# Kernel optimization log

Hardware: AMD Instinct MI355X
Metric: run time of the kernel (lower is better)

## Reference

```python
import jax, jax.numpy as jnp
import numpy as np

EPS = 1e-6
SIGMA = 0.5          # observation_noise_std
E, B, M, C = 64, 512, 128, 128  # episode, batch, memory_size, code_size


def setup_inputs() -> dict:
    key = jax.random.key(0)
    k1, k2 = jax.random.split(key)
    return {
        "input_encoded": jax.random.normal(k1, (E, B, C), dtype=jnp.float32),
        "memory_mean": jax.random.normal(k2, (M, C), dtype=jnp.float32),
        "memory_logvar": jnp.zeros((1,), dtype=jnp.float32),
    }


def reference(input_encoded, memory_mean, memory_logvar):
    # GPM.write_to_memory with direct_writing=False (sequential Kalman write).
    bsz = input_encoded.shape[1]
    prior_var = jnp.exp(memory_logvar) * jnp.ones((M,), input_encoded.dtype) + EPS  # (M,)
    prior_mean = jnp.broadcast_to(memory_mean, (bsz, M, C))                # (B,M,C)
    prior_cov = jnp.broadcast_to(jnp.diag(prior_var), (bsz, M, M))         # (B,M,M)
    eye_m = jnp.eye(M, dtype=input_encoded.dtype)

    def step(carry, z_i):            # z_i: (B,C)
        mean, cov = carry            # (B,M,C), (B,M,M)
        # _solve_w_mean (pseudoinverse=False): w = inv(M M^T + s^2 I) M z
        gram = jnp.einsum('bmc,bnc->bmn', mean, mean) + (SIGMA ** 2) * eye_m
        mz = jnp.einsum('bmc,bc->bm', mean, z_i)
        w = jnp.linalg.solve(gram, mz[..., None])[..., 0]  # (B,M)
        # _update_memory: rank-1 Kalman update
        delta = z_i - jnp.einsum('bm,bmc->bc', w, mean)    # (B,C)
        wU = jnp.einsum('bm,bmn->bn', w, cov)              # (B,M)
        sig = jnp.sum(wU * w, axis=-1) + SIGMA ** 2        # (B,)
        c = wU / sig[:, None]                              # (B,M)
        new_mean = mean + c[:, :, None] * delta[:, None, :]
        new_cov = cov - c[:, :, None] * wU[:, None, :]
        return (new_mean, new_cov), None

    (post_mean, post_cov), _ = jax.lax.scan(step, (prior_mean, prior_cov), input_encoded)

    # _dkl_M
    p_diag = jnp.diagonal(prior_cov, axis1=-2, axis2=-1)   # (B,M)
    q_diag = jnp.diagonal(post_cov, axis1=-2, axis2=-1)    # (B,M)
    t1 = C * jnp.sum(q_diag / p_diag, axis=-1)
    t2 = jnp.sum((post_mean - prior_mean) ** 2 / p_diag[..., None], axis=(-2, -1))
    t3 = -C * M
    t4 = C * jnp.sum(jnp.log(p_diag) - jnp.log(q_diag), axis=-1)
    dkl_M = jnp.mean(t1 + t2 + t3 + t4)
    return post_mean, post_cov, dkl_M
```

## Files before the change

kernel.cpp:

```cpp
#include <hip/hip_runtime.h>
#include <math.h>

#define MM   128
#define CC   128
#define EE   64
#define BB   512
#define LDT  132
#define SIG2 0.25f
#define SIG4 0.0625f
#define EPSV 1e-6f

#define AT_OFF   0
#define U_OFF    (128*LDT)
#define VEC_BASE (2*128*LDT)
#define VEC(i)   (VEC_BASE + (i)*128)
#define SC_OFF   (VEC_BASE + 7*128)
#define SMEM_FLOATS (SC_OFF + 24)
#define SMEM_BYTES  (SMEM_FLOATS * 4)

#define KATTR __attribute__((amdgpu_flat_work_group_size(512, 512), amdgpu_waves_per_eu(1, 2)))

__device__ __forceinline__ void ginv_inplace(float* sm, const int t) {
    float* T   = sm + AT_OFF;
    float* piv = sm + SC_OFF + 22;
    const int rg = t >> 2, cq = t & 3, ccb = cq << 5;
    float Gacc[32];
    #pragma unroll
    for (int j = 0; j < 32; ++j) Gacc[j] = 0.f;
    #pragma unroll 1
    for (int cc = 0; cc < 32; ++cc) {
        const float4 ar = *(const float4*)&T[rg*LDT + 4*cc];
        #pragma unroll
        for (int j = 0; j < 32; ++j) {
            const float4 br = *(const float4*)&T[(ccb + j)*LDT + 4*cc];
            Gacc[j] += ar.x*br.x + ar.y*br.y + ar.z*br.z + ar.w*br.w;
        }
    }
    #pragma unroll
    for (int j = 0; j < 32; ++j)
        if (ccb + j == rg) Gacc[j] += SIG2;
    __syncthreads();
    #pragma unroll
    for (int j4 = 0; j4 < 8; ++j4) {
        float4 v; v.x = Gacc[4*j4]; v.y = Gacc[4*j4+1]; v.z = Gacc[4*j4+2]; v.w = Gacc[4*j4+3];
        *(float4*)&T[rg*LDT + ccb + 4*j4] = v;
    }
    #pragma unroll 1
    for (int k = 0; k < 128; ++k) {
        const int kq = k >> 5;
        __syncthreads();
        if (rg == k && cq == kq) piv[0] = 1.0f / T[k*LDT + k];
        __syncthreads();
        if (rg == k) {
            const float pinv = piv[0];
            #pragma unroll
            for (int j4 = 0; j4 < 8; ++j4) {
                float4 g = *(float4*)&T[k*LDT + ccb + 4*j4];
                g.x *= pinv; g.y *= pinv; g.z *= pinv; g.w *= pinv;
                *(float4*)&T[k*LDT + ccb + 4*j4] = g;
            }
            if (cq == kq) T[k*LDT + k] = pinv;
        }
        __syncthreads();
        const float f = (rg == k) ? 0.f : T[rg*LDT + k];
        __syncthreads();
        if (rg != k) {
            #pragma unroll
            for (int j4 = 0; j4 < 8; ++j4) {
                float4 own = *(float4*)&T[rg*LDT + ccb + 4*j4];
                const float4 pv = *(const float4*)&T[k*LDT + ccb + 4*j4];
                own.x -= f*pv.x; own.y -= f*pv.y; own.z -= f*pv.z; own.w -= f*pv.w;
                *(float4*)&T[rg*LDT + ccb + 4*j4] = own;
            }
            if (cq == kq) T[rg*LDT + k] -= f;
        }
    }
    __syncthreads();
}

__global__ KATTR void gpm_setup(const float* __restrict__ mean0,
                                float* __restrict__ ginv0) {
    extern __shared__ float sm[];
    float* T = sm + AT_OFF;
    const int t = threadIdx.x;
    const int rg = t >> 2, cq = t & 3, ccb = cq << 5;
    const float* src = mean0 + rg*CC + ccb;
    #pragma unroll
    for (int j4 = 0; j4 < 8; ++j4)
        *(float4*)&T[rg*LDT + ccb + 4*j4] = *(const float4*)&src[4*j4];
    __syncthreads();
    ginv_inplace(sm, t);
    #pragma unroll
    for (int j4 = 0; j4 < 8; ++j4)
        *(float4*)&ginv0[rg*CC + ccb + 4*j4] = *(const float4*)&T[rg*LDT + ccb + 4*j4];
}

#define SC_ADD(slot, val) { float v_ = (val);                                 \
    v_ += __shfl_xor(v_, 1, 64); v_ += __shfl_xor(v_, 2, 64);                 \
    v_ += __shfl_xor(v_, 4, 64);                                              \
    if ((l & 7) == 0) atomicAdd(&scal[slot], v_); }

__global__ KATTR void gpm_main(
        const float* __restrict__ zin, const float* __restrict__ mean0,
        const float* __restrict__ lvar, float* __restrict__ out,
        const float* __restrict__ ginv0, const int use_ws) {
    extern __shared__ float sm[];
    float* At  = sm + AT_OFF;
    float* U   = sm + U_OFF;
    float* vz  = sm + VEC(0);
    float* vaz = sm + VEC(1);
    float* vw0 = sm + VEC(2);
    float* vt2 = sm + VEC(3);
    float* vuw = sm + VEC(4);
    float* vg1 = sm + VEC(5);
    float* vg2 = sm + VEC(6);
    float* scal = sm + SC_OFF;

    const int t = threadIdx.x, b = blockIdx.x;
    const int w = t >> 6, l = t & 63;
    const int r  = ((w & 1) << 6) | l;
    const int q  = w >> 1;
    const int cb = q << 5;

    sm[VEC(1) + t] = 0.f;
    if (t < 256) sm[VEC(1) + 512 + t] = 0.f;
    if (t < 24)  scal[t] = 0.f;

    const float pvar = expf(lvar[0]) + EPSV;

    float Areg[32], Greg[32];

    if (use_ws) {
        const float* src = ginv0 + r*CC + cb;
        #pragma unroll
        for (int j4 = 0; j4 < 8; ++j4) {
            const float4 v = *(const float4*)&src[4*j4];
            Greg[4*j4] = v.x; Greg[4*j4+1] = v.y; Greg[4*j4+2] = v.z; Greg[4*j4+3] = v.w;
        }
    } else {
        const float* src = mean0 + r*CC + cb;
        #pragma unroll
        for (int j4 = 0; j4 < 8; ++j4)
            *(float4*)&At[r*LDT + cb + 4*j4] = *(const float4*)&src[4*j4];
        __syncthreads();
        ginv_inplace(sm, t);
        #pragma unroll
        for (int j4 = 0; j4 < 8; ++j4) {
            const float4 v = *(const float4*)&At[r*LDT + cb + 4*j4];
            Greg[4*j4] = v.x; Greg[4*j4+1] = v.y; Greg[4*j4+2] = v.z; Greg[4*j4+3] = v.w;
        }
        __syncthreads();
    }
    {
        const float* src = mean0 + r*CC + cb;
        #pragma unroll
        for (int j4 = 0; j4 < 8; ++j4) {
            const float4 v = *(const float4*)&src[4*j4];
            Areg[4*j4] = v.x; Areg[4*j4+1] = v.y; Areg[4*j4+2] = v.z; Areg[4*j4+3] = v.w;
        }
    }
    {
        const float4 z4 = {0.f, 0.f, 0.f, 0.f};
        #pragma unroll
        for (int j4 = 0; j4 < 8; ++j4)
            *(float4*)&U[r*LDT + cb + 4*j4] = z4;
        if (r >= cb && r < cb + 32) U[r*LDT + r] = pvar;
    }
    #pragma unroll
    for (int j = 0; j < 32; ++j) At[(cb + j)*LDT + r] = Areg[j];
    if (t < 32)
        *(float4*)&vz[4*t] = *(const float4*)&zin[(size_t)b*CC + 4*t];
    __syncthreads();

    {
        float s = 0.f;
        #pragma unroll
        for (int j4 = 0; j4 < 8; ++j4) {
            const float4 x = *(const float4*)&vz[cb + 4*j4];
            s += Areg[4*j4]*x.x + Areg[4*j4+1]*x.y + Areg[4*j4+2]*x.z + Areg[4*j4+3]*x.w;
        }
        atomicAdd(&vaz[r], s);
    }
    __syncthreads();

    #pragma unroll 1
    for (int e = 0; e < EE; ++e) {
        {
            float s = 0.f;
            #pragma unroll
            for (int j4 = 0; j4 < 8; ++j4) {
                const float4 x = *(const float4*)&vaz[cb + 4*j4];
                s += Greg[4*j4]*x.x + Greg[4*j4+1]*x.y + Greg[4*j4+2]*x.z + Greg[4*j4+3]*x.w;
            }
            atomicAdd(&vw0[r], s);
            if (t < 128) vt2[t] = vz[t];
            if (t < 384) (sm + VEC(4))[t] = 0.f;
            if (t == 448) { scal[0] = SIG2; scal[1] = 0.f; scal[2] = 0.f; scal[3] = 0.f; scal[4] = 0.f; }
        }
        __syncthreads();
        {
            float s1 = 0.f, s2 = 0.f, s3 = 0.f;
            #pragma unroll
            for (int j4 = 0; j4 < 8; ++j4) {
                const float4 a = *(const float4*)&At[r*LDT + cb + 4*j4];
                const float4 u = *(const float4*)&U[r*LDT + cb + 4*j4];
                const float4 x = *(const float4*)&vw0[cb + 4*j4];
                s1 += a.x*x.x + a.y*x.y + a.z*x.z + a.w*x.w;
                s2 += u.x*x.x + u.y*x.y + u.z*x.z + u.w*x.w;
                s3 += Greg[4*j4]*x.x + Greg[4*j4+1]*x.y + Greg[4*j4+2]*x.z + Greg[4*j4+3]*x.w;
            }
            atomicAdd(&vt2[r], -s1);
            atomicAdd(&vuw[r], s2);
            atomicAdd(&vg1[r], s3);
            const float w_r = vw0[r];
            SC_ADD(0, s2 * w_r);
            SC_ADD(3, s3 * w_r);
            if (t < 128) vaz[t] = 0.f;
        }
        __syncthreads();
        {
            float s = 0.f;
            #pragma unroll
            for (int j4 = 0; j4 < 8; ++j4) {
                const float4 x = *(const float4*)&vuw[cb + 4*j4];
                s += Greg[4*j4]*x.x + Greg[4*j4+1]*x.y + Greg[4*j4+2]*x.z + Greg[4*j4+3]*x.w;
            }
            atomicAdd(&vg2[r], s);
            SC_ADD(2, s * vuw[r]);
            if (t < 128) {
                float d_ = vt2[t]; d_ *= d_;
                d_ += __shfl_xor(d_, 1, 64); d_ += __shfl_xor(d_, 2, 64); d_ += __shfl_xor(d_, 4, 64);
                if ((l & 7) == 0) atomicAdd(&scal[1], d_);
                float p_ = vg1[t] * vuw[t];
                p_ += __shfl_xor(p_, 1, 64); p_ += __shfl_xor(p_, 2, 64); p_ += __shfl_xor(p_, 4, 64);
                if ((l & 7) == 0) atomicAdd(&scal[4], p_);
                vw0[t] = 0.f;
            }
            if (t < 32 && e + 1 < EE)
                *(float4*)&vz[4*t] = *(const float4*)&zin[((size_t)(e+1)*BB + b)*CC + 4*t];
        }
        __syncthreads();
        {
            const float sig = scal[0];
            const float inv_sig = 1.0f / sig;
            const float d2v = scal[1];
            const float s_uwg2 = scal[2];
            const float s_vg1  = SIG4 * scal[3];
            const float s_uwg1 = SIG2 * scal[4];
            const float b11 = s_vg1 - d2v;
            const float b12 = 1.0f + s_uwg1*inv_sig;
            const float b22 = s_uwg2*inv_sig*inv_sig;
            const float idet = 1.0f / (b11*b22 - b12*b12);
            const float K11 = b22*idet, K12v = -b12*idet, K22 = b11*idet;
            const float k12s = K12v*inv_sig, k22s = K22*inv_sig*inv_sig;
            const float cr  = vuw[r]*inv_sig;
            const float g1r = SIG2 * vg1[r];
            const float g2r = vg2[r];
            const float ar_ = K11*g1r + k12s*g2r;
            const float br_ = k12s*g1r + k22s*g2r;
            const float ars = ar_ * SIG2;
            #pragma unroll
            for (int j4 = 0; j4 < 8; ++j4) {
                const float4 dd = *(const float4*)&vt2[cb + 4*j4];
                Areg[4*j4]   += cr*dd.x; Areg[4*j4+1] += cr*dd.y;
                Areg[4*j4+2] += cr*dd.z; Areg[4*j4+3] += cr*dd.w;
                const float4 uu = *(const float4*)&vuw[cb + 4*j4];
                float4 u = *(float4*)&U[r*LDT + cb + 4*j4];
                u.x -= cr*uu.x; u.y -= cr*uu.y; u.z -= cr*uu.z; u.w -= cr*uu.w;
                *(float4*)&U[r*LDT + cb + 4*j4] = u;
                const float4 q1 = *(const float4*)&vg1[cb + 4*j4];
                const float4 q2 = *(const float4*)&vg2[cb + 4*j4];
                Greg[4*j4]   -= ars*q1.x + br_*q2.x;
                Greg[4*j4+1] -= ars*q1.y + br_*q2.y;
                Greg[4*j4+2] -= ars*q1.z + br_*q2.z;
                Greg[4*j4+3] -= ars*q1.w + br_*q2.w;
            }
            #pragma unroll
            for (int j = 0; j < 32; ++j) At[(cb + j)*LDT + r] = Areg[j];
            if (e + 1 < EE) {
                float s = 0.f;
                #pragma unroll
                for (int j4 = 0; j4 < 8; ++j4) {
                    const float4 x = *(const float4*)&vz[cb + 4*j4];
                    s += Areg[4*j4]*x.x + Areg[4*j4+1]*x.y + Areg[4*j4+2]*x.z + Areg[4*j4+3]*x.w;
                }
                atomicAdd(&vaz[r], s);
            }
        }
        __syncthreads();
    }

    {
        float* dst = out + (size_t)b*(MM*CC) + r*CC + cb;
        #pragma unroll
        for (int j4 = 0; j4 < 8; ++j4) {
            float4 v; v.x = Areg[4*j4]; v.y = Areg[4*j4+1]; v.z = Areg[4*j4+2]; v.w = Areg[4*j4+3];
            *(float4*)&dst[4*j4] = v;
        }
    }
    {
        float* dst = out + (size_t)BB*(MM*CC) + (size_t)b*(MM*MM) + r*MM + cb;
        #pragma unroll
        for (int j4 = 0; j4 < 8; ++j4)
            *(float4*)&dst[4*j4] = *(const float4*)&U[r*LDT + cb + 4*j4];
    }
    {
        const float inv_p = 1.0f / pvar;
        float acc = 0.f;
        const float* src = mean0 + r*CC + cb;
        #pragma unroll
        for (int j4 = 0; j4 < 8; ++j4) {
            const float4 a0 = *(const float4*)&src[4*j4];
            const float dx = Areg[4*j4]   - a0.x, dy = Areg[4*j4+1] - a0.y;
            const float dz = Areg[4*j4+2] - a0.z, dw = Areg[4*j4+3] - a0.w;
            acc += dx*dx + dy*dy + dz*dz + dw*dw;
        }
        float local = acc * inv_p;
        if (q == (r >> 5)) {
            const float qd = U[r*LDT + r];
            local += (float)CC * (qd*inv_p + logf(pvar) - logf(qd));
        }
        #pragma unroll
        for (int m2 = 1; m2 < 64; m2 <<= 1) local += __shfl_xor(local, m2, 64);
        if (l == 0) scal[6 + w] = local;
        __syncthreads();
        if (t == 0) {
            float tot = 0.f;
            #pragma unroll
            for (int i = 0; i < 8; ++i) tot += scal[6 + i];
            tot -= (float)(CC*MM);
            atomicAdd(out + (size_t)2*BB*MM*CC, tot * (1.0f/(float)BB));
        }
    }
}

extern "C" void kernel_launch(void* const* d_in, const int* in_sizes, int n_in,
                              void* d_out, int out_size, void* d_ws, size_t ws_size,
                              hipStream_t stream) {
    (void)in_sizes; (void)n_in; (void)out_size;
    const float* zin   = (const float*)d_in[0];
    const float* mean0 = (const float*)d_in[1];
    const float* lvar  = (const float*)d_in[2];
    float* out = (float*)d_out;
    float* dkl = out + (size_t)2*BB*MM*CC;
    const int use_ws = (d_ws != nullptr && ws_size >= (size_t)MM*MM*4) ? 1 : 0;
    float* ginv0 = (float*)d_ws;

    hipFuncSetAttribute((const void*)gpm_setup, hipFuncAttributeMaxDynamicSharedMemorySize, SMEM_BYTES);
    hipFuncSetAttribute((const void*)gpm_main,  hipFuncAttributeMaxDynamicSharedMemorySize, SMEM_BYTES);

    hipMemsetAsync(dkl, 0, sizeof(float), stream);
    if (use_ws)
        gpm_setup<<<1, 512, SMEM_BYTES, stream>>>(mean0, ginv0);
    gpm_main<<<BB, 512, SMEM_BYTES, stream>>>(zin, mean0, lvar, out, ginv0, use_ws);
}
```

Measured before the change: 1.465 ms.

## Defer inverse-Gram update to next step with double-buffered vectors to drop a barrier

Result: faster. 1.367 ms (-6.6%).

```diff
diff --git a/kernel.cpp b/kernel.cpp
--- a/kernel.cpp
+++ b/kernel.cpp
@@ -14,15 +14,15 @@
 #define U_OFF    (128*LDT)
 #define VEC_BASE (2*128*LDT)
 #define VEC(i)   (VEC_BASE + (i)*128)
-#define SC_OFF   (VEC_BASE + 7*128)
-#define SMEM_FLOATS (SC_OFF + 24)
+#define SC_OFF   (VEC_BASE + 9*128)
+#define SMEM_FLOATS (SC_OFF + 32)
 #define SMEM_BYTES  (SMEM_FLOATS * 4)
 
 #define KATTR __attribute__((amdgpu_flat_work_group_size(512, 512), amdgpu_waves_per_eu(1, 2)))
 
 __device__ __forceinline__ void ginv_inplace(float* sm, const int t) {
     float* T   = sm + AT_OFF;
-    float* piv = sm + SC_OFF + 22;
+    float* piv = sm + SC_OFF + 30;
     const int rg = t >> 2, cq = t & 3, ccb = cq << 5;
     float Gacc[32];
     #pragma unroll
@@ -95,10 +95,10 @@
         *(float4*)&ginv0[rg*CC + ccb + 4*j4] = *(const float4*)&T[rg*LDT + ccb + 4*j4];
 }
 
-#define SC_ADD(slot, val) { float v_ = (val);                                 \
+#define SC_ADD(base, slot, val) { float v_ = (val);                           \
     v_ += __shfl_xor(v_, 1, 64); v_ += __shfl_xor(v_, 2, 64);                 \
     v_ += __shfl_xor(v_, 4, 64);                                              \
-    if ((l & 7) == 0) atomicAdd(&scal[slot], v_); }
+    if ((l & 7) == 0) atomicAdd(&(base)[slot], v_); }
 
 __global__ KATTR void gpm_main(
         const float* __restrict__ zin, const float* __restrict__ mean0,
@@ -112,8 +112,6 @@
     float* vw0 = sm + VEC(2);
     float* vt2 = sm + VEC(3);
     float* vuw = sm + VEC(4);
-    float* vg1 = sm + VEC(5);
-    float* vg2 = sm + VEC(6);
     float* scal = sm + SC_OFF;
 
     const int t = threadIdx.x, b = blockIdx.x;
@@ -123,8 +121,9 @@
     const int cb = q << 5;
 
     sm[VEC(1) + t] = 0.f;
-    if (t < 256) sm[VEC(1) + 512 + t] = 0.f;
-    if (t < 24)  scal[t] = 0.f;
+    sm[VEC(1) + 512 + t] = 0.f;
+    if (t < 32) scal[t] = 0.f;
+    if (t == 0) { scal[0] = SIG2; scal[8] = SIG2; }
 
     const float pvar = expf(lvar[0]) + EPSV;
 
@@ -185,17 +184,46 @@
 
     #pragma unroll 1
     for (int e = 0; e < EE; ++e) {
+        const int p  = e & 1;
+        const int pp = p ^ 1;
+        float* g1p = sm + VEC(5) + (p  << 7);
+        float* g1q = sm + VEC(5) + (pp << 7);
+        float* g2p = sm + VEC(7) + (p  << 7);
+        float* g2q = sm + VEC(7) + (pp << 7);
+        float* scp = scal + 8*p;
+        float* scq = scal + 8*pp;
         {
+            const float sigp    = scq[0];
+            const float inv_sig = 1.0f / sigp;
+            const float d2v     = scq[1];
+            const float s_uwg2  = scq[2];
+            const float s_vg1   = SIG4 * scq[3];
+            const float s_uwg1  = SIG2 * scq[4];
+            const float b11  = s_vg1 - d2v;
+            const float b12  = 1.0f + s_uwg1*inv_sig;
+            const float b22  = s_uwg2*inv_sig*inv_sig;
+            const float idet = 1.0f / (b11*b22 - b12*b12);
+            const float K11 = b22*idet, K12v = -b12*idet, K22 = b11*idet;
+            const float k12s = K12v*inv_sig, k22s = K22*inv_sig*inv_sig;
+            const float g1r = SIG2 * g1q[r];
+            const float g2r = g2q[r];
+            const float ar_ = K11*g1r + k12s*g2r;
+            const float br_ = k12s*g1r + k22s*g2r;
+            const float ars = ar_ * SIG2;
             float s = 0.f;
             #pragma unroll
             for (int j4 = 0; j4 < 8; ++j4) {
+                const float4 q1 = *(const float4*)&g1q[cb + 4*j4];
+                const float4 q2 = *(const float4*)&g2q[cb + 4*j4];
+                Greg[4*j4]   -= ars*q1.x + br_*q2.x;
+                Greg[4*j4+1] -= ars*q1.y + br_*q2.y;
+                Greg[4*j4+2] -= ars*q1.z + br_*q2.z;
+                Greg[4*j4+3] -= ars*q1.w + br_*q2.w;
                 const float4 x = *(const float4*)&vaz[cb + 4*j4];
                 s += Greg[4*j4]*x.x + Greg[4*j4+1]*x.y + Greg[4*j4+2]*x.z + Greg[4*j4+3]*x.w;
             }
             atomicAdd(&vw0[r], s);
-            if (t < 128) vt2[t] = vz[t];
-            if (t < 384) (sm + VEC(4))[t] = 0.f;
-            if (t == 448) { scal[0] = SIG2; scal[1] = 0.f; scal[2] = 0.f; scal[3] = 0.f; scal[4] = 0.f; }
+            if (t < 128) { vt2[t] = vz[t]; vuw[t] = 0.f; }
         }
         __syncthreads();
         {
@@ -211,11 +239,14 @@
             }
             atomicAdd(&vt2[r], -s1);
             atomicAdd(&vuw[r], s2);
-            atomicAdd(&vg1[r], s3);
+            atomicAdd(&g1p[r], s3);
             const float w_r = vw0[r];
-            SC_ADD(0, s2 * w_r);
-            SC_ADD(3, s3 * w_r);
-            if (t < 128) vaz[t] = 0.f;
+            SC_ADD(scp, 0, s2 * w_r);
+            SC_ADD(scp, 3, s3 * w_r);
+            if (t < 128) { g1q[t] = 0.f; g2q[t] = 0.f; vaz[t] = 0.f; }
+            if (t == 448) { scq[0] = SIG2; scq[1] = 0.f; scq[2] = 0.f; scq[3] = 0.f; scq[4] = 0.f; }
+            if (t < 32 && e + 1 < EE)
+                *(float4*)&vz[4*t] = *(const float4*)&zin[((size_t)(e+1)*BB + b)*CC + 4*t];
         }
         __syncthreads();
         {
@@ -225,40 +256,20 @@
                 const float4 x = *(const float4*)&vuw[cb + 4*j4];
                 s += Greg[4*j4]*x.x + Greg[4*j4+1]*x.y + Greg[4*j4+2]*x.z + Greg[4*j4+3]*x.w;
             }
-            atomicAdd(&vg2[r], s);
-            SC_ADD(2, s * vuw[r]);
+            atomicAdd(&g2p[r], s);
+            SC_ADD(scp, 2, s * vuw[r]);
             if (t < 128) {
                 float d_ = vt2[t]; d_ *= d_;
                 d_ += __shfl_xor(d_, 1, 64); d_ += __shfl_xor(d_, 2, 64); d_ += __shfl_xor(d_, 4, 64);
-                if ((l & 7) == 0) atomicAdd(&scal[1], d_);
-                float p_ = vg1[t] * vuw[t];
+                if ((l & 7) == 0) atomicAdd(&scp[1], d_);
+                float p_ = g1p[t] * vuw[t];
                 p_ += __shfl_xor(p_, 1, 64); p_ += __shfl_xor(p_, 2, 64); p_ += __shfl_xor(p_, 4, 64);
-                if ((l & 7) == 0) atomicAdd(&scal[4], p_);
+                if ((l & 7) == 0) atomicAdd(&scp[4], p_);
                 vw0[t] = 0.f;
             }
-            if (t < 32 && e + 1 < EE)
-                *(float4*)&vz[4*t] = *(const float4*)&zin[((size_t)(e+1)*BB + b)*CC + 4*t];
-        }
-        __syncthreads();
-        {
-            const float sig = scal[0];
+            const float sig = scp[0];
             const float inv_sig = 1.0f / sig;
-            const float d2v = scal[1];
-            const float s_uwg2 = scal[2];
-            const float s_vg1  = SIG4 * scal[3];
-            const float s_uwg1 = SIG2 * scal[4];
-            const float b11 = s_vg1 - d2v;
-            const float b12 = 1.0f + s_uwg1*inv_sig;
-            const float b22 = s_uwg2*inv_sig*inv_sig;
-            const float idet = 1.0f / (b11*b22 - b12*b12);
-            const float K11 = b22*idet, K12v = -b12*idet, K22 = b11*idet;
-            const float k12s = K12v*inv_sig, k22s = K22*inv_sig*inv_sig;
-            const float cr  = vuw[r]*inv_sig;
-            const float g1r = SIG2 * vg1[r];
-            const float g2r = vg2[r];
-            const float ar_ = K11*g1r + k12s*g2r;
-            const float br_ = k12s*g1r + k22s*g2r;
-            const float ars = ar_ * SIG2;
+            const float cr = vuw[r] * inv_sig;
             #pragma unroll
             for (int j4 = 0; j4 < 8; ++j4) {
                 const float4 dd = *(const float4*)&vt2[cb + 4*j4];
@@ -268,23 +279,17 @@
                 float4 u = *(float4*)&U[r*LDT + cb + 4*j4];
                 u.x -= cr*uu.x; u.y -= cr*uu.y; u.z -= cr*uu.z; u.w -= cr*uu.w;
                 *(float4*)&U[r*LDT + cb + 4*j4] = u;
-                const float4 q1 = *(const float4*)&vg1[cb + 4*j4];
-                const float4 q2 = *(const float4*)&vg2[cb + 4*j4];
-                Greg[4*j4]   -= ars*q1.x + br_*q2.x;
-                Greg[4*j4+1] -= ars*q1.y + br_*q2.y;
-                Greg[4*j4+2] -= ars*q1.z + br_*q2.z;
-                Greg[4*j4+3] -= ars*q1.w + br_*q2.w;
             }
             #pragma unroll
             for (int j = 0; j < 32; ++j) At[(cb + j)*LDT + r] = Areg[j];
             if (e + 1 < EE) {
-                float s = 0.f;
+                float s2 = 0.f;
                 #pragma unroll
                 for (int j4 = 0; j4 < 8; ++j4) {
                     const float4 x = *(const float4*)&vz[cb + 4*j4];
-                    s += Areg[4*j4]*x.x + Areg[4*j4+1]*x.y + Areg[4*j4+2]*x.z + Areg[4*j4+3]*x.w;
+                    s2 += Areg[4*j4]*x.x + Areg[4*j4+1]*x.y + Areg[4*j4+2]*x.z + Areg[4*j4+3]*x.w;
                 }
-                atomicAdd(&vaz[r], s);
+                atomicAdd(&vaz[r], s2);
             }
         }
         __syncthreads();
@@ -322,12 +327,12 @@
         }
         #pragma unroll
         for (int m2 = 1; m2 < 64; m2 <<= 1) local += __shfl_xor(local, m2, 64);
-        if (l == 0) scal[6 + w] = local;
+        if (l == 0) scal[16 + w] = local;
         __syncthreads();
         if (t == 0) {
             float tot = 0.f;
             #pragma unroll
-            for (int i = 0; i < 8; ++i) tot += scal[6 + i];
+            for (int i = 0; i < 8; ++i) tot += scal[16 + i];
             tot -= (float)(CC*MM);
             atomicAdd(out + (size_t)2*BB*MM*CC, tot * (1.0f/(float)BB));
         }
```
